# Optimization experiments

Hardware: AMD Instinct MI355X
Metric: run time of the kernel (lower is better)

Reference implementation:

```python
import jax, jax.numpy as jnp
import numpy as np
from math import ceil, log2

LEVELS = 8
# pywt 'db4' filters (length 8)
DB4_DEC_HI = np.array([-0.23037781330885523, 0.7148465705525415, -0.6308807679295904,
                       -0.02798376941698385, 0.18703481171888114, 0.030841381835986965,
                       -0.032883011666982945, -0.010597401784997278], dtype=np.float32)
DB4_REC_HI = np.array([-0.010597401784997278, -0.032883011666982945, 0.030841381835986965,
                       0.18703481171888114, -0.02798376941698385, -0.6308807679295904,
                       0.7148465705525415, -0.23037781330885523], dtype=np.float32)


def setup_inputs() -> dict:
    key = jax.random.key(0)
    x = jax.random.normal(key, (2048, 3000), dtype=jnp.float32)
    scaling = jnp.tile(jnp.asarray(DB4_DEC_HI), (LEVELS, 1))       # [levels, 8]
    scaling_rec = jnp.tile(jnp.asarray(DB4_REC_HI), (LEVELS, 1))   # [levels, 8]
    return {"input": x, "scaling": scaling, "scaling_rec": scaling_rec}


def _make_wavelet(h):
    # g = flip(h); g[1::2] *= -1
    g = jnp.flip(h, axis=-1)
    signs = jnp.where(jnp.arange(g.shape[-1]) % 2 == 1, -1.0, 1.0).astype(g.dtype)
    return g * signs


def _circ_conv(x, filt, transpose=False):
    # FFT-based circular convolution (filter zero-padded to input length)
    L = x.shape[-1]
    ra = jnp.fft.rfft(x)
    rb = jnp.fft.rfft(filt, n=L)
    if transpose:
        rb = jnp.conj(rb)
    return jnp.fft.irfft(ra * rb, n=L)


def _upsample2(x):
    # interleave zeros: out[:, ::2] = x
    n, k = x.shape
    out = jnp.zeros((n, 2 * k), dtype=x.dtype)
    return out.at[:, ::2].set(x)


def _forward(x, scaling, scaling_rec):
    levels = scaling.shape[0]
    m = x.shape[1]
    L = 2 ** ceil(log2(m))
    p0 = (L - m) // 2
    p1 = ceil((L - m) / 2)
    x = jnp.pad(x, ((0, 0), (p0, p1)), mode="edge")  # ReplicationPad1d

    approx = x
    wav_coeffs = []
    for lvl in range(levels):
        wavelet = _make_wavelet(scaling_rec[lvl])
        details = _circ_conv(approx, wavelet)[:, ::2]
        approx = _circ_conv(approx, scaling[lvl])[:, ::2]
        wav_coeffs.append(details)
    wav_coeffs.append(approx)

    # (no thresholding: the original forward copies coeffs unmodified)
    filtered = list(wav_coeffs)
    approx = filtered[-1]
    for lvl in reversed(range(levels)):
        details = filtered[lvl]
        wav_syn = _make_wavelet(scaling_rec[lvl])
        d_rec = _circ_conv(_upsample2(details), wav_syn, transpose=True)
        a_rec = _circ_conv(_upsample2(approx), scaling[lvl], transpose=True)
        approx = d_rec + a_rec

    recon = approx[:, p0:m + p1]
    coeffs = jnp.concatenate(wav_coeffs, axis=-1)  # total length == L
    return recon, coeffs


def reference(input, scaling, scaling_rec):
    return _forward(input, scaling, scaling_rec)
```

## Files before the change

kernel.cpp:

```cpp
#include <hip/hip_runtime.h>

#define NROWS 2048
#define MLEN  3000
#define LPAD  4096
#define PAD0  548
#define NLVL  8
#define NT    256

union F4 { float4 v; float f[4]; };

__device__ inline void lds_barrier() {
    asm volatile("s_waitcnt lgkmcnt(0)\n\ts_barrier" ::: "memory");
}

__global__ __launch_bounds__(NT, 8) void despawn_kernel(
    const float* __restrict__ x,
    const float* __restrict__ scaling,
    const float* __restrict__ scaling_rec,
    float* __restrict__ recon_out,
    float* __restrict__ coef_out)
{
    __shared__ __align__(16) float SA[2048];
    __shared__ __align__(16) float SB[2176];
    __shared__ __align__(16) float CS[512];
    __shared__ float fsca[64];
    __shared__ float fwav[64];

    const int tid = threadIdx.x;
    const int row = blockIdx.x;
    float* const crow = coef_out + (size_t)row * LPAD;
    const float* xr = x + (size_t)row * MLEN;

    {
        const int lag = (blockIdx.x >> 3) & 3;
        for (int i = 0; i < lag; ++i) __builtin_amdgcn_s_sleep(8);
    }

    if (tid < 64) {
        const int lvl = tid >> 3, k = tid & 7;
        fsca[tid] = scaling[tid];
        fwav[tid] = scaling_rec[lvl * 8 + (7 - k)] * ((k & 1) ? -1.0f : 1.0f);
    }

    for (int h = 0; h < 2; ++h) {
        const int j0 = 1024 * h;
        for (int gi = tid; gi < 514; gi += NT) {
            const int n0 = 2 * j0 - 8 + 4 * gi;
            F4 u;
            if (n0 >= PAD0 && n0 + 3 <= PAD0 + MLEN - 1) {
                u.v = *reinterpret_cast<const float4*>(xr + (n0 - PAD0));
            } else {
#pragma unroll
                for (int e = 0; e < 4; ++e) {
                    int n = n0 + e;
                    if (n < 0) n += LPAD;
                    int g = n - PAD0;
                    g = g < 0 ? 0 : (g > MLEN - 1 ? MLEN - 1 : g);
                    u.f[e] = xr[g];
                }
            }
            *reinterpret_cast<float2*>(&SB[2 * gi])        = make_float2(u.f[0], u.f[2]);
            *reinterpret_cast<float2*>(&SB[1088 + 2 * gi]) = make_float2(u.f[1], u.f[3]);
        }
        lds_barrier();
        {
            float W[8], S[8];
#pragma unroll
            for (int k = 0; k < 8; ++k) { W[k] = fwav[k]; S[k] = fsca[k]; }
            const float4* ev4 = reinterpret_cast<const float4*>(&SB[0]);
            const float4* od4 = reinterpret_cast<const float4*>(&SB[1088]);
            float4* dst4 = reinterpret_cast<float4*>(crow + j0);
            const int t = tid;
            F4 Ea, Eb, Oa, Ob;
            Ea.v = ev4[t];
            Eb.v = ev4[t + 1];
            Oa.v = od4[t];
            Ob.v = od4[t + 1];
            float e[8] = {Ea.f[0],Ea.f[1],Ea.f[2],Ea.f[3],Eb.f[0],Eb.f[1],Eb.f[2],Eb.f[3]};
            float o[8] = {Oa.f[0],Oa.f[1],Oa.f[2],Oa.f[3],Ob.f[0],Ob.f[1],Ob.f[2],Ob.f[3]};
            float ds[4], as[4];
#pragma unroll
            for (int u = 0; u < 4; ++u) {
                float d = 0.f, a = 0.f;
#pragma unroll
                for (int m = 0; m < 4; ++m) {
                    const float vE = e[4 + u - m];
                    const float vO = o[3 + u - m];
                    d = fmaf(vE, W[2 * m], d);
                    d = fmaf(vO, W[2 * m + 1], d);
                    a = fmaf(vE, S[2 * m], a);
                    a = fmaf(vO, S[2 * m + 1], a);
                }
                ds[u] = d; as[u] = a;
            }
            F4 dv; dv.f[0] = ds[0]; dv.f[1] = ds[1]; dv.f[2] = ds[2]; dv.f[3] = ds[3];
            dst4[t] = dv.v;
            *reinterpret_cast<float2*>(SA + (j0 >> 1) + 2 * t)        = make_float2(as[0], as[2]);
            *reinterpret_cast<float2*>(SA + 1024 + (j0 >> 1) + 2 * t) = make_float2(as[1], as[3]);
        }
        lds_barrier();
    }

    {
        float* cur = SA;
        float* alt = SB;
        int H = 1024;
        int coff = 2048;
        for (int lvl = 1; lvl < NLVL; ++lvl) {
            float W[8], S[8];
#pragma unroll
            for (int k = 0; k < 8; ++k) { W[k] = fwav[lvl * 8 + k]; S[k] = fsca[lvl * 8 + k]; }
            const int q = H >> 2;
            const int qm = q - 1;
            const float4* ev4 = reinterpret_cast<const float4*>(cur);
            const float4* od4 = reinterpret_cast<const float4*>(cur + H);
            float4* dst4 = reinterpret_cast<float4*>(crow + coff);
            float4* mir4 = (lvl == 1) ? reinterpret_cast<float4*>(&SB[1088])
                         : (lvl == 2) ? reinterpret_cast<float4*>(&SA[512])
                                      : reinterpret_cast<float4*>(&CS[coff - 3584]);
            for (int t = tid; t < q; t += NT) {
                F4 Ea, Eb, Oa, Ob;
                Ea.v = ev4[(t - 1) & qm];
                Eb.v = ev4[t];
                Oa.v = od4[(t - 1) & qm];
                Ob.v = od4[t];
                float e[8] = {Ea.f[0],Ea.f[1],Ea.f[2],Ea.f[3],Eb.f[0],Eb.f[1],Eb.f[2],Eb.f[3]};
                float o[8] = {Oa.f[0],Oa.f[1],Oa.f[2],Oa.f[3],Ob.f[0],Ob.f[1],Ob.f[2],Ob.f[3]};
                float ds[4], as[4];
#pragma unroll
                for (int u = 0; u < 4; ++u) {
                    float d = 0.f, a = 0.f;
#pragma unroll
                    for (int m = 0; m < 4; ++m) {
                        const float vE = e[4 + u - m];
                        const float vO = o[3 + u - m];
                        d = fmaf(vE, W[2 * m], d);
                        d = fmaf(vO, W[2 * m + 1], d);
                        a = fmaf(vE, S[2 * m], a);
                        a = fmaf(vO, S[2 * m + 1], a);
                    }
                    ds[u] = d; as[u] = a;
                }
                F4 dv; dv.f[0] = ds[0]; dv.f[1] = ds[1]; dv.f[2] = ds[2]; dv.f[3] = ds[3];
                dst4[t] = dv.v;
                mir4[t] = dv.v;
                *reinterpret_cast<float2*>(alt + 2 * t)            = make_float2(as[0], as[2]);
                *reinterpret_cast<float2*>(alt + (H >> 1) + 2 * t) = make_float2(as[1], as[3]);
            }
            lds_barrier();
            coff += H;
            float* tmp = cur; cur = alt; alt = tmp;
            H >>= 1;
        }
    }

    if (tid < 16) {
        const float v = SB[((tid & 1) ? 8 : 0) + (tid >> 1)];
        crow[LPAD - 16 + tid] = v;
        CS[496 + tid] = v;
    }
    __syncthreads();

    const float* a = &CS[496];
    float* obuf = SA;
    int len = 16;
    for (int lvl = NLVL - 1; lvl >= 1; --lvl) {
        float W[8], S[8];
#pragma unroll
        for (int k = 0; k < 8; ++k) { W[k] = fwav[lvl * 8 + k]; S[k] = fsca[lvl * 8 + k]; }
        const int Mout = len << 1;
        const int doff = LPAD - (LPAD >> lvl);
        const float4* d4 = (lvl >= 3) ? reinterpret_cast<const float4*>(&CS[doff - 3584])
                         : (lvl == 2) ? reinterpret_cast<const float4*>(&SA[512])
                                      : reinterpret_cast<const float4*>(&SB[1088]);
        const float4* a4 = reinterpret_cast<const float4*>(a);
        const int gq = Mout >> 3;
        const int fm = (len >> 2) - 1;
        for (int g = tid; g < gq; g += NT) {
            F4 Da, Db, Aa, Ab;
            Da.v = d4[g]; Db.v = d4[(g + 1) & fm];
            Aa.v = a4[g]; Ab.v = a4[(g + 1) & fm];
            float dd[8] = {Da.f[0],Da.f[1],Da.f[2],Da.f[3],Db.f[0],Db.f[1],Db.f[2],Db.f[3]};
            float aa[8] = {Aa.f[0],Aa.f[1],Aa.f[2],Aa.f[3],Ab.f[0],Ab.f[1],Ab.f[2],Ab.f[3]};
            float out[8];
#pragma unroll
            for (int u = 0; u < 8; ++u) {
                const int p = u & 1, c = (u + 1) >> 1;
                float s = 0.f;
#pragma unroll
                for (int m = 0; m < 4; ++m) {
                    s = fmaf(dd[c + m], W[p + 2 * m], s);
                    s = fmaf(aa[c + m], S[p + 2 * m], s);
                }
                out[u] = s;
            }
            F4 o0, o1;
            o0.f[0] = out[0]; o0.f[1] = out[1]; o0.f[2] = out[2]; o0.f[3] = out[3];
            o1.f[0] = out[4]; o1.f[1] = out[5]; o1.f[2] = out[6]; o1.f[3] = out[7];
            float4* ob4 = reinterpret_cast<float4*>(obuf + 8 * g);
            ob4[0] = o0.v; ob4[1] = o1.v;
        }
        lds_barrier();
        a = obuf;
        obuf = (obuf == SA) ? SB : SA;
        len = Mout;
    }

    {
        float W[8], S[8];
#pragma unroll
        for (int k = 0; k < 8; ++k) { W[k] = fwav[k]; S[k] = fsca[k]; }
        const float4* d4 = reinterpret_cast<const float4*>(crow);
        const float4* a4 = reinterpret_cast<const float4*>(a);
        const int fm = (len >> 2) - 1;
        float* const ro = recon_out + (size_t)row * MLEN;
        for (int g = tid; g < (LPAD >> 3); g += NT) {
            F4 Da, Db, Aa, Ab;
            Da.v = d4[g]; Db.v = d4[(g + 1) & fm];
            Aa.v = a4[g]; Ab.v = a4[(g + 1) & fm];
            float dd[8] = {Da.f[0],Da.f[1],Da.f[2],Da.f[3],Db.f[0],Db.f[1],Db.f[2],Db.f[3]};
            float aa[8] = {Aa.f[0],Aa.f[1],Aa.f[2],Aa.f[3],Ab.f[0],Ab.f[1],Ab.f[2],Ab.f[3]};
            float out[8];
#pragma unroll
            for (int u = 0; u < 8; ++u) {
                const int p = u & 1, c = (u + 1) >> 1;
                float s = 0.f;
#pragma unroll
                for (int m = 0; m < 4; ++m) {
                    s = fmaf(dd[c + m], W[p + 2 * m], s);
                    s = fmaf(aa[c + m], S[p + 2 * m], s);
                }
                out[u] = s;
            }
            const int n0 = 8 * g;
            if (n0 >= PAD0 && n0 + 8 <= PAD0 + MLEN) {
                F4 o0, o1;
                o0.f[0] = out[0]; o0.f[1] = out[1]; o0.f[2] = out[2]; o0.f[3] = out[3];
                o1.f[0] = out[4]; o1.f[1] = out[5]; o1.f[2] = out[6]; o1.f[3] = out[7];
                float4* r4 = reinterpret_cast<float4*>(ro + (n0 - PAD0));
                r4[0] = o0.v; r4[1] = o1.v;
            } else {
#pragma unroll
                for (int u = 0; u < 8; ++u) {
                    const int n = n0 + u;
                    if (n >= PAD0 && n < PAD0 + MLEN) ro[n - PAD0] = out[u];
                }
            }
        }
    }
}

extern "C" void kernel_launch(void* const* d_in, const int* in_sizes, int n_in,
                              void* d_out, int out_size, void* d_ws, size_t ws_size,
                              hipStream_t stream) {
    const float* x           = (const float*)d_in[0];
    const float* scaling     = (const float*)d_in[1];
    const float* scaling_rec = (const float*)d_in[2];
    float* recon = (float*)d_out;
    float* coefo = recon + (size_t)NROWS * MLEN;
    despawn_kernel<<<dim3(NROWS), dim3(NT), 0, stream>>>(x, scaling, scaling_rec,
                                                         recon, coefo);
    (void)in_sizes; (void)n_in; (void)out_size; (void)d_ws; (void)ws_size;
}
```

Before: 99.39 us.

## Process two rows per block to amortize barriers and filter loads

Each block now handles two rows, with per-row LDS buffers, and every stage loop is unrolled over both rows. This halves the number of blocks and shares barriers and filter-coefficient loads across the two rows. At the deep levels with few active threads it also doubles the useful work per barrier. The staggered start sleep is removed and launch bounds drop to 4 blocks per CU, because LDS use per block roughly doubles. That lowers the number of resident waves and may hurt latency hiding.

```diff
diff --git a/kernel.cpp b/kernel.cpp
--- a/kernel.cpp
+++ b/kernel.cpp
@@ -6,6 +6,7 @@
 #define PAD0  548
 #define NLVL  8
 #define NT    256
+#define RPB   2
 
 union F4 { float4 v; float f[4]; };
 
@@ -13,27 +14,27 @@
     asm volatile("s_waitcnt lgkmcnt(0)\n\ts_barrier" ::: "memory");
 }
 
-__global__ __launch_bounds__(NT, 8) void despawn_kernel(
+__global__ __launch_bounds__(NT, 4) void despawn_kernel(
     const float* __restrict__ x,
     const float* __restrict__ scaling,
     const float* __restrict__ scaling_rec,
     float* __restrict__ recon_out,
     float* __restrict__ coef_out)
 {
-    __shared__ __align__(16) float SA[2048];
-    __shared__ __align__(16) float SB[2176];
-    __shared__ __align__(16) float CS[512];
+    __shared__ __align__(16) float SA[RPB][2048];
+    __shared__ __align__(16) float SB[RPB][2176];
+    __shared__ __align__(16) float CS[RPB][512];
     __shared__ float fsca[64];
     __shared__ float fwav[64];
 
     const int tid = threadIdx.x;
-    const int row = blockIdx.x;
-    float* const crow = coef_out + (size_t)row * LPAD;
-    const float* xr = x + (size_t)row * MLEN;
-
-    {
-        const int lag = (blockIdx.x >> 3) & 3;
-        for (int i = 0; i < lag; ++i) __builtin_amdgcn_s_sleep(8);
+    const int row0 = blockIdx.x * RPB;
+    const float* xr[RPB];
+    float* crow[RPB];
+#pragma unroll
+    for (int r = 0; r < RPB; ++r) {
+        xr[r] = x + (size_t)(row0 + r) * MLEN;
+        crow[r] = coef_out + (size_t)(row0 + r) * LPAD;
     }
 
     if (tid < 64) {
@@ -46,84 +47,40 @@
         const int j0 = 1024 * h;
         for (int gi = tid; gi < 514; gi += NT) {
             const int n0 = 2 * j0 - 8 + 4 * gi;
-            F4 u;
-            if (n0 >= PAD0 && n0 + 3 <= PAD0 + MLEN - 1) {
-                u.v = *reinterpret_cast<const float4*>(xr + (n0 - PAD0));
-            } else {
-#pragma unroll
-                for (int e = 0; e < 4; ++e) {
-                    int n = n0 + e;
-                    if (n < 0) n += LPAD;
-                    int g = n - PAD0;
-                    g = g < 0 ? 0 : (g > MLEN - 1 ? MLEN - 1 : g);
-                    u.f[e] = xr[g];
-                }
-            }
-            *reinterpret_cast<float2*>(&SB[2 * gi])        = make_float2(u.f[0], u.f[2]);
-            *reinterpret_cast<float2*>(&SB[1088 + 2 * gi]) = make_float2(u.f[1], u.f[3]);
+#pragma unroll
+            for (int r = 0; r < RPB; ++r) {
+                F4 u;
+                if (n0 >= PAD0 && n0 + 3 <= PAD0 + MLEN - 1) {
+                    u.v = *reinterpret_cast<const float4*>(xr[r] + (n0 - PAD0));
+                } else {
+#pragma unroll
+                    for (int e = 0; e < 4; ++e) {
+                        int n = n0 + e;
+                        if (n < 0) n += LPAD;
+                        int g = n - PAD0;
+                        g = g < 0 ? 0 : (g > MLEN - 1 ? MLEN - 1 : g);
+                        u.f[e] = xr[r][g];
+                    }
+                }
+                *reinterpret_cast<float2*>(&SB[r][2 * gi])        = make_float2(u.f[0], u.f[2]);
+                *reinterpret_cast<float2*>(&SB[r][1088 + 2 * gi]) = make_float2(u.f[1], u.f[3]);
+            }
         }
         lds_barrier();
         {
             float W[8], S[8];
 #pragma unroll
             for (int k = 0; k < 8; ++k) { W[k] = fwav[k]; S[k] = fsca[k]; }
-            const float4* ev4 = reinterpret_cast<const float4*>(&SB[0]);
-            const float4* od4 = reinterpret_cast<const float4*>(&SB[1088]);
-            float4* dst4 = reinterpret_cast<float4*>(crow + j0);
             const int t = tid;
-            F4 Ea, Eb, Oa, Ob;
-            Ea.v = ev4[t];
-            Eb.v = ev4[t + 1];
-            Oa.v = od4[t];
-            Ob.v = od4[t + 1];
-            float e[8] = {Ea.f[0],Ea.f[1],Ea.f[2],Ea.f[3],Eb.f[0],Eb.f[1],Eb.f[2],Eb.f[3]};
-            float o[8] = {Oa.f[0],Oa.f[1],Oa.f[2],Oa.f[3],Ob.f[0],Ob.f[1],Ob.f[2],Ob.f[3]};
-            float ds[4], as[4];
-#pragma unroll
-            for (int u = 0; u < 4; ++u) {
-                float d = 0.f, a = 0.f;
-#pragma unroll
-                for (int m = 0; m < 4; ++m) {
-                    const float vE = e[4 + u - m];
-                    const float vO = o[3 + u - m];
-                    d = fmaf(vE, W[2 * m], d);
-                    d = fmaf(vO, W[2 * m + 1], d);
-                    a = fmaf(vE, S[2 * m], a);
-                    a = fmaf(vO, S[2 * m + 1], a);
-                }
-                ds[u] = d; as[u] = a;
-            }
-            F4 dv; dv.f[0] = ds[0]; dv.f[1] = ds[1]; dv.f[2] = ds[2]; dv.f[3] = ds[3];
-            dst4[t] = dv.v;
-            *reinterpret_cast<float2*>(SA + (j0 >> 1) + 2 * t)        = make_float2(as[0], as[2]);
-            *reinterpret_cast<float2*>(SA + 1024 + (j0 >> 1) + 2 * t) = make_float2(as[1], as[3]);
-        }
-        lds_barrier();
-    }
-
-    {
-        float* cur = SA;
-        float* alt = SB;
-        int H = 1024;
-        int coff = 2048;
-        for (int lvl = 1; lvl < NLVL; ++lvl) {
-            float W[8], S[8];
-#pragma unroll
-            for (int k = 0; k < 8; ++k) { W[k] = fwav[lvl * 8 + k]; S[k] = fsca[lvl * 8 + k]; }
-            const int q = H >> 2;
-            const int qm = q - 1;
-            const float4* ev4 = reinterpret_cast<const float4*>(cur);
-            const float4* od4 = reinterpret_cast<const float4*>(cur + H);
-            float4* dst4 = reinterpret_cast<float4*>(crow + coff);
-            float4* mir4 = (lvl == 1) ? reinterpret_cast<float4*>(&SB[1088])
-                         : (lvl == 2) ? reinterpret_cast<float4*>(&SA[512])
-                                      : reinterpret_cast<float4*>(&CS[coff - 3584]);
-            for (int t = tid; t < q; t += NT) {
+#pragma unroll
+            for (int r = 0; r < RPB; ++r) {
+                const float4* ev4 = reinterpret_cast<const float4*>(&SB[r][0]);
+                const float4* od4 = reinterpret_cast<const float4*>(&SB[r][1088]);
                 F4 Ea, Eb, Oa, Ob;
-                Ea.v = ev4[(t - 1) & qm];
-                Eb.v = ev4[t];
-                Oa.v = od4[(t - 1) & qm];
-                Ob.v = od4[t];
+                Ea.v = ev4[t];
+                Eb.v = ev4[t + 1];
+                Oa.v = od4[t];
+                Ob.v = od4[t + 1];
                 float e[8] = {Ea.f[0],Ea.f[1],Ea.f[2],Ea.f[3],Eb.f[0],Eb.f[1],Eb.f[2],Eb.f[3]};
                 float o[8] = {Oa.f[0],Oa.f[1],Oa.f[2],Oa.f[3],Ob.f[0],Ob.f[1],Ob.f[2],Ob.f[3]};
                 float ds[4], as[4];
@@ -142,108 +99,173 @@
                     ds[u] = d; as[u] = a;
                 }
                 F4 dv; dv.f[0] = ds[0]; dv.f[1] = ds[1]; dv.f[2] = ds[2]; dv.f[3] = ds[3];
-                dst4[t] = dv.v;
-                mir4[t] = dv.v;
-                *reinterpret_cast<float2*>(alt + 2 * t)            = make_float2(as[0], as[2]);
-                *reinterpret_cast<float2*>(alt + (H >> 1) + 2 * t) = make_float2(as[1], as[3]);
+                reinterpret_cast<float4*>(crow[r] + j0)[t] = dv.v;
+                *reinterpret_cast<float2*>(&SA[r][(j0 >> 1) + 2 * t])        = make_float2(as[0], as[2]);
+                *reinterpret_cast<float2*>(&SA[r][1024 + (j0 >> 1) + 2 * t]) = make_float2(as[1], as[3]);
+            }
+        }
+        lds_barrier();
+    }
+
+    {
+        int curA = 1;
+        int H = 1024;
+        int coff = 2048;
+        for (int lvl = 1; lvl < NLVL; ++lvl) {
+            float W[8], S[8];
+#pragma unroll
+            for (int k = 0; k < 8; ++k) { W[k] = fwav[lvl * 8 + k]; S[k] = fsca[lvl * 8 + k]; }
+            const int q = H >> 2;
+            const int qm = q - 1;
+            for (int t = tid; t < q; t += NT) {
+#pragma unroll
+                for (int r = 0; r < RPB; ++r) {
+                    float* cur = curA ? &SA[r][0] : &SB[r][0];
+                    float* alt = curA ? &SB[r][0] : &SA[r][0];
+                    float* mir = (lvl == 1) ? &SB[r][1088]
+                               : (lvl == 2) ? &SA[r][512]
+                                            : &CS[r][coff - 3584];
+                    const float4* ev4 = reinterpret_cast<const float4*>(cur);
+                    const float4* od4 = reinterpret_cast<const float4*>(cur + H);
+                    F4 Ea, Eb, Oa, Ob;
+                    Ea.v = ev4[(t - 1) & qm];
+                    Eb.v = ev4[t];
+                    Oa.v = od4[(t - 1) & qm];
+                    Ob.v = od4[t];
+                    float e[8] = {Ea.f[0],Ea.f[1],Ea.f[2],Ea.f[3],Eb.f[0],Eb.f[1],Eb.f[2],Eb.f[3]};
+                    float o[8] = {Oa.f[0],Oa.f[1],Oa.f[2],Oa.f[3],Ob.f[0],Ob.f[1],Ob.f[2],Ob.f[3]};
+                    float ds[4], as[4];
+#pragma unroll
+                    for (int u = 0; u < 4; ++u) {
+                        float d = 0.f, a = 0.f;
+#pragma unroll
+                        for (int m = 0; m < 4; ++m) {
+                            const float vE = e[4 + u - m];
+                            const float vO = o[3 + u - m];
+                            d = fmaf(vE, W[2 * m], d);
+                            d = fmaf(vO, W[2 * m + 1], d);
+                            a = fmaf(vE, S[2 * m], a);
+                            a = fmaf(vO, S[2 * m + 1], a);
+                        }
+                        ds[u] = d; as[u] = a;
+                    }
+                    F4 dv; dv.f[0] = ds[0]; dv.f[1] = ds[1]; dv.f[2] = ds[2]; dv.f[3] = ds[3];
+                    reinterpret_cast<float4*>(crow[r] + coff)[t] = dv.v;
+                    reinterpret_cast<float4*>(mir)[t] = dv.v;
+                    *reinterpret_cast<float2*>(alt + 2 * t)            = make_float2(as[0], as[2]);
+                    *reinterpret_cast<float2*>(alt + (H >> 1) + 2 * t) = make_float2(as[1], as[3]);
+                }
             }
             lds_barrier();
             coff += H;
-            float* tmp = cur; cur = alt; alt = tmp;
+            curA ^= 1;
             H >>= 1;
         }
     }
 
     if (tid < 16) {
-        const float v = SB[((tid & 1) ? 8 : 0) + (tid >> 1)];
-        crow[LPAD - 16 + tid] = v;
-        CS[496 + tid] = v;
+#pragma unroll
+        for (int r = 0; r < RPB; ++r) {
+            const float v = SB[r][((tid & 1) ? 8 : 0) + (tid >> 1)];
+            crow[r][LPAD - 16 + tid] = v;
+            CS[r][496 + tid] = v;
+        }
     }
     __syncthreads();
 
-    const float* a = &CS[496];
-    float* obuf = SA;
-    int len = 16;
-    for (int lvl = NLVL - 1; lvl >= 1; --lvl) {
-        float W[8], S[8];
-#pragma unroll
-        for (int k = 0; k < 8; ++k) { W[k] = fwav[lvl * 8 + k]; S[k] = fsca[lvl * 8 + k]; }
-        const int Mout = len << 1;
-        const int doff = LPAD - (LPAD >> lvl);
-        const float4* d4 = (lvl >= 3) ? reinterpret_cast<const float4*>(&CS[doff - 3584])
-                         : (lvl == 2) ? reinterpret_cast<const float4*>(&SA[512])
-                                      : reinterpret_cast<const float4*>(&SB[1088]);
-        const float4* a4 = reinterpret_cast<const float4*>(a);
-        const int gq = Mout >> 3;
-        const int fm = (len >> 2) - 1;
-        for (int g = tid; g < gq; g += NT) {
-            F4 Da, Db, Aa, Ab;
-            Da.v = d4[g]; Db.v = d4[(g + 1) & fm];
-            Aa.v = a4[g]; Ab.v = a4[(g + 1) & fm];
-            float dd[8] = {Da.f[0],Da.f[1],Da.f[2],Da.f[3],Db.f[0],Db.f[1],Db.f[2],Db.f[3]};
-            float aa[8] = {Aa.f[0],Aa.f[1],Aa.f[2],Aa.f[3],Ab.f[0],Ab.f[1],Ab.f[2],Ab.f[3]};
-            float out[8];
-#pragma unroll
-            for (int u = 0; u < 8; ++u) {
-                const int p = u & 1, c = (u + 1) >> 1;
-                float s = 0.f;
-#pragma unroll
-                for (int m = 0; m < 4; ++m) {
-                    s = fmaf(dd[c + m], W[p + 2 * m], s);
-                    s = fmaf(aa[c + m], S[p + 2 * m], s);
-                }
-                out[u] = s;
-            }
-            F4 o0, o1;
-            o0.f[0] = out[0]; o0.f[1] = out[1]; o0.f[2] = out[2]; o0.f[3] = out[3];
-            o1.f[0] = out[4]; o1.f[1] = out[5]; o1.f[2] = out[6]; o1.f[3] = out[7];
-            float4* ob4 = reinterpret_cast<float4*>(obuf + 8 * g);
-            ob4[0] = o0.v; ob4[1] = o1.v;
-        }
-        lds_barrier();
-        a = obuf;
-        obuf = (obuf == SA) ? SB : SA;
-        len = Mout;
+    {
+        int aIsCS = 1;
+        int obufA = 1;
+        int len = 16;
+        for (int lvl = NLVL - 1; lvl >= 1; --lvl) {
+            float W[8], S[8];
+#pragma unroll
+            for (int k = 0; k < 8; ++k) { W[k] = fwav[lvl * 8 + k]; S[k] = fsca[lvl * 8 + k]; }
+            const int Mout = len << 1;
+            const int doff = LPAD - (LPAD >> lvl);
+            const int gq = Mout >> 3;
+            const int fm = (len >> 2) - 1;
+            for (int g = tid; g < gq; g += NT) {
+#pragma unroll
+                for (int r = 0; r < RPB; ++r) {
+                    const float4* d4 = (lvl >= 3) ? reinterpret_cast<const float4*>(&CS[r][doff - 3584])
+                                     : (lvl == 2) ? reinterpret_cast<const float4*>(&SA[r][512])
+                                                  : reinterpret_cast<const float4*>(&SB[r][1088]);
+                    const float* ap = aIsCS ? &CS[r][496] : (obufA ? &SB[r][0] : &SA[r][0]);
+                    const float4* a4 = reinterpret_cast<const float4*>(ap);
+                    float* obuf = obufA ? &SA[r][0] : &SB[r][0];
+                    F4 Da, Db, Aa, Ab;
+                    Da.v = d4[g]; Db.v = d4[(g + 1) & fm];
+                    Aa.v = a4[g]; Ab.v = a4[(g + 1) & fm];
+                    float dd[8] = {Da.f[0],Da.f[1],Da.f[2],Da.f[3],Db.f[0],Db.f[1],Db.f[2],Db.f[3]};
+                    float aa[8] = {Aa.f[0],Aa.f[1],Aa.f[2],Aa.f[3],Ab.f[0],Ab.f[1],Ab.f[2],Ab.f[3]};
+                    float out[8];
+#pragma unroll
+                    for (int u = 0; u < 8; ++u) {
+                        const int p = u & 1, c = (u + 1) >> 1;
+                        float s = 0.f;
+#pragma unroll
+                        for (int m = 0; m < 4; ++m) {
+                            s = fmaf(dd[c + m], W[p + 2 * m], s);
+                            s = fmaf(aa[c + m], S[p + 2 * m], s);
+                        }
+                        out[u] = s;
+                    }
+                    F4 o0, o1;
+                    o0.f[0] = out[0]; o0.f[1] = out[1]; o0.f[2] = out[2]; o0.f[3] = out[3];
+                    o1.f[0] = out[4]; o1.f[1] = out[5]; o1.f[2] = out[6]; o1.f[3] = out[7];
+                    float4* ob4 = reinterpret_cast<float4*>(obuf + 8 * g);
+                    ob4[0] = o0.v; ob4[1] = o1.v;
+                }
+            }
+            lds_barrier();
+            aIsCS = 0;
+            obufA ^= 1;
+            len = Mout;
+        }
     }
 
     {
         float W[8], S[8];
 #pragma unroll
         for (int k = 0; k < 8; ++k) { W[k] = fwav[k]; S[k] = fsca[k]; }
-        const float4* d4 = reinterpret_cast<const float4*>(crow);
-        const float4* a4 = reinterpret_cast<const float4*>(a);
-        const int fm = (len >> 2) - 1;
-        float* const ro = recon_out + (size_t)row * MLEN;
+        const int fm = (2048 >> 2) - 1;
         for (int g = tid; g < (LPAD >> 3); g += NT) {
-            F4 Da, Db, Aa, Ab;
-            Da.v = d4[g]; Db.v = d4[(g + 1) & fm];
-            Aa.v = a4[g]; Ab.v = a4[(g + 1) & fm];
-            float dd[8] = {Da.f[0],Da.f[1],Da.f[2],Da.f[3],Db.f[0],Db.f[1],Db.f[2],Db.f[3]};
-            float aa[8] = {Aa.f[0],Aa.f[1],Aa.f[2],Aa.f[3],Ab.f[0],Ab.f[1],Ab.f[2],Ab.f[3]};
-            float out[8];
-#pragma unroll
-            for (int u = 0; u < 8; ++u) {
-                const int p = u & 1, c = (u + 1) >> 1;
-                float s = 0.f;
-#pragma unroll
-                for (int m = 0; m < 4; ++m) {
-                    s = fmaf(dd[c + m], W[p + 2 * m], s);
-                    s = fmaf(aa[c + m], S[p + 2 * m], s);
-                }
-                out[u] = s;
-            }
             const int n0 = 8 * g;
-            if (n0 >= PAD0 && n0 + 8 <= PAD0 + MLEN) {
-                F4 o0, o1;
-                o0.f[0] = out[0]; o0.f[1] = out[1]; o0.f[2] = out[2]; o0.f[3] = out[3];
-                o1.f[0] = out[4]; o1.f[1] = out[5]; o1.f[2] = out[6]; o1.f[3] = out[7];
-                float4* r4 = reinterpret_cast<float4*>(ro + (n0 - PAD0));
-                r4[0] = o0.v; r4[1] = o1.v;
-            } else {
+#pragma unroll
+            for (int r = 0; r < RPB; ++r) {
+                const float4* d4 = reinterpret_cast<const float4*>(crow[r]);
+                const float4* a4 = reinterpret_cast<const float4*>(&SA[r][0]);
+                float* const ro = recon_out + (size_t)(row0 + r) * MLEN;
+                F4 Da, Db, Aa, Ab;
+                Da.v = d4[g]; Db.v = d4[(g + 1) & fm];
+                Aa.v = a4[g]; Ab.v = a4[(g + 1) & fm];
+                float dd[8] = {Da.f[0],Da.f[1],Da.f[2],Da.f[3],Db.f[0],Db.f[1],Db.f[2],Db.f[3]};
+                float aa[8] = {Aa.f[0],Aa.f[1],Aa.f[2],Aa.f[3],Ab.f[0],Ab.f[1],Ab.f[2],Ab.f[3]};
+                float out[8];
 #pragma unroll
                 for (int u = 0; u < 8; ++u) {
-                    const int n = n0 + u;
-                    if (n >= PAD0 && n < PAD0 + MLEN) ro[n - PAD0] = out[u];
+                    const int p = u & 1, c = (u + 1) >> 1;
+                    float s = 0.f;
+#pragma unroll
+                    for (int m = 0; m < 4; ++m) {
+                        s = fmaf(dd[c + m], W[p + 2 * m], s);
+                        s = fmaf(aa[c + m], S[p + 2 * m], s);
+                    }
+                    out[u] = s;
+                }
+                if (n0 >= PAD0 && n0 + 8 <= PAD0 + MLEN) {
+                    F4 o0, o1;
+                    o0.f[0] = out[0]; o0.f[1] = out[1]; o0.f[2] = out[2]; o0.f[3] = out[3];
+                    o1.f[0] = out[4]; o1.f[1] = out[5]; o1.f[2] = out[6]; o1.f[3] = out[7];
+                    float4* r4 = reinterpret_cast<float4*>(ro + (n0 - PAD0));
+                    r4[0] = o0.v; r4[1] = o1.v;
+                } else {
+#pragma unroll
+                    for (int u = 0; u < 8; ++u) {
+                        const int n = n0 + u;
+                        if (n >= PAD0 && n < PAD0 + MLEN) ro[n - PAD0] = out[u];
+                    }
                 }
             }
         }
@@ -258,7 +280,7 @@
     const float* scaling_rec = (const float*)d_in[2];
     float* recon = (float*)d_out;
     float* coefo = recon + (size_t)NROWS * MLEN;
-    despawn_kernel<<<dim3(NROWS), dim3(NT), 0, stream>>>(x, scaling, scaling_rec,
-                                                         recon, coefo);
+    despawn_kernel<<<dim3(NROWS / RPB), dim3(NT), 0, stream>>>(x, scaling, scaling_rec,
+                                                               recon, coefo);
     (void)in_sizes; (void)n_in; (void)out_size; (void)d_ws; (void)ws_size;
 }
```

Result: no change. 100.2 us (+0.8%).
